# Kernel optimization log

Measured on AMD Instinct MI355X. Metric: run time of the kernel, lower is better.

## Reference

```python
import jax, jax.numpy as jnp
import numpy as np

K = 5  # kernel_size
B, N, H, Wd = 2, 8, 512, 512

def setup_inputs() -> dict:
    key = jax.random.key(0)
    k1, k2, k3 = jax.random.split(key, 3)
    frames = jax.random.normal(k1, (B, N, H, Wd), dtype=jnp.float32)
    core = jax.random.normal(k2, (B, N * K * K, H, Wd), dtype=jnp.float32)
    W = jax.random.uniform(k3, (B, N, H, Wd), dtype=jnp.float32)
    return {"frames": frames, "core": core, "W": W}

def reference(frames, core, W):
    b, n, h, w = frames.shape
    p = K // 2
    # pad spatial dims
    fp = jnp.pad(frames, ((0, 0), (0, 0), (p, p), (p, p)))
    # K^2 shifted views -> [B, N, K^2, H, W] (mirrors torch stack order i-major)
    patches = jnp.stack([fp[..., i:i + h, j:j + w] for i in range(K) for j in range(K)], axis=2)
    # split+stack of core along channels == reshape to [B, N, K^2, H, W]
    c = core.reshape(b, n, K * K, h, w)
    pred = jnp.sum(c * patches, axis=2)  # per-pixel dynamic conv
    return W * pred
```

## Files before the change

kernel.cpp:

```cpp
#include <hip/hip_runtime.h>


#define KK   5
#define PADR 2
#define BB   2
#define NN   8
#define HH   512
#define WW   512

constexpr int SROW    = WW + 2 * PADR;
constexpr int SSTRIDE = SROW + 4;

__global__ __launch_bounds__(128) void kpn_kernel(
    const float* __restrict__ frames,
    const float* __restrict__ core,
    const float* __restrict__ Wt,
    float* __restrict__ out)
{
    __shared__ float smem[KK * SSTRIDE];

    const int tid = threadIdx.x;
    const int h   = blockIdx.x % HH;
    const int bn  = blockIdx.x / HH;

    const float* fbase = frames + (size_t)bn * HH * WW;
    #pragma unroll
    for (int i = 0; i < KK; ++i) {
        const int  row = h - PADR + i;
        const bool rok = (row >= 0) && (row < HH);
        const float* frow = fbase + (size_t)row * WW;
        for (int idx = tid; idx < SROW; idx += 128) {
            const int x = idx - PADR;
            float v = 0.0f;
            if (rok && x >= 0 && x < WW) v = frow[x];
            smem[i * SSTRIDE + idx] = v;
        }
    }
    __syncthreads();

    const int w0 = tid * 4;

    float fr[KK][8];
    #pragma unroll
    for (int i = 0; i < KK; ++i) {
        #pragma unroll
        for (int t = 0; t < 8; ++t)
            fr[i][t] = smem[i * SSTRIDE + w0 + t];
    }

    float acc0 = 0.f, acc1 = 0.f, acc2 = 0.f, acc3 = 0.f;

    const float* cbase = core + ((size_t)bn * (KK * KK) * HH + h) * WW + w0;
    #pragma unroll
    for (int i = 0; i < KK; ++i) {
        #pragma unroll
        for (int j = 0; j < KK; ++j) {
            const int c = i * KK + j;
            const float4 cv = *(const float4*)(cbase + (size_t)c * HH * WW);
            acc0 += cv.x * fr[i][j + 0];
            acc1 += cv.y * fr[i][j + 1];
            acc2 += cv.z * fr[i][j + 2];
            acc3 += cv.w * fr[i][j + 3];
        }
    }

    const size_t o  = ((size_t)bn * HH + h) * WW + w0;
    const float4 wv = *(const float4*)(Wt + o);
    float4 ov;
    ov.x = wv.x * acc0;
    ov.y = wv.y * acc1;
    ov.z = wv.z * acc2;
    ov.w = wv.w * acc3;
    *(float4*)(out + o) = ov;
}

extern "C" void kernel_launch(void* const* d_in, const int* in_sizes, int n_in,
                              void* d_out, int out_size, void* d_ws, size_t ws_size,
                              hipStream_t stream)
{
    const float* frames = (const float*)d_in[0];
    const float* core   = (const float*)d_in[1];
    const float* Wt     = (const float*)d_in[2];
    float*       out    = (float*)d_out;

    const dim3 grid(BB * NN * HH);
    kpn_kernel<<<grid, 128, 0, stream>>>(frames, core, Wt, out);
}
```

Measured before the change: 569.2 us.

## Drop shared-memory staging; load frame halo directly with vector loads and nontemporal hints

Removes the shared-memory tile and barrier. Each thread now reads its own 8-wide halo per row straight from global memory using vector loads, so neighbouring threads' reads overlap and are served by cache. Streaming core and W reads and the output write use nontemporal loads and stores to reduce cache pollution. The grid becomes 2D, which removes the div/mod on the block index. The kernel is dominated by the core read bandwidth, so any gain is likely small. Redundant halo reads add some L1/L2 traffic.

```diff
diff --git a/kernel.cpp b/kernel.cpp
--- a/kernel.cpp
+++ b/kernel.cpp
@@ -2,14 +2,13 @@
 
 
 #define KK   5
-#define PADR 2
 #define BB   2
 #define NN   8
 #define HH   512
 #define WW   512
 
-constexpr int SROW    = WW + 2 * PADR;
-constexpr int SSTRIDE = SROW + 4;
+typedef float  v4f __attribute__((ext_vector_type(4)));
+typedef float  v2f __attribute__((ext_vector_type(2)));
 
 __global__ __launch_bounds__(128) void kpn_kernel(
     const float* __restrict__ frames,
@@ -17,61 +16,56 @@
     const float* __restrict__ Wt,
     float* __restrict__ out)
 {
-    __shared__ float smem[KK * SSTRIDE];
+    const int tid = threadIdx.x;
+    const int h   = blockIdx.x;
+    const int bn  = blockIdx.y;
+    const int w0  = tid * 4;
 
-    const int tid = threadIdx.x;
-    const int h   = blockIdx.x % HH;
-    const int bn  = blockIdx.x / HH;
+    const bool has_left  = (tid != 0);
+    const bool has_right = (tid != 127);
 
     const float* fbase = frames + (size_t)bn * HH * WW;
-    #pragma unroll
-    for (int i = 0; i < KK; ++i) {
-        const int  row = h - PADR + i;
-        const bool rok = (row >= 0) && (row < HH);
-        const float* frow = fbase + (size_t)row * WW;
-        for (int idx = tid; idx < SROW; idx += 128) {
-            const int x = idx - PADR;
-            float v = 0.0f;
-            if (rok && x >= 0 && x < WW) v = frow[x];
-            smem[i * SSTRIDE + idx] = v;
-        }
-    }
-    __syncthreads();
-
-    const int w0 = tid * 4;
-
-    float fr[KK][8];
-    #pragma unroll
-    for (int i = 0; i < KK; ++i) {
-        #pragma unroll
-        for (int t = 0; t < 8; ++t)
-            fr[i][t] = smem[i * SSTRIDE + w0 + t];
-    }
 
     float acc0 = 0.f, acc1 = 0.f, acc2 = 0.f, acc3 = 0.f;
 
     const float* cbase = core + ((size_t)bn * (KK * KK) * HH + h) * WW + w0;
+
     #pragma unroll
     for (int i = 0; i < KK; ++i) {
+        const int  r   = h - 2 + i;
+        const bool rok = (r >= 0) && (r < HH);
+        const float* rp = fbase + (size_t)r * WW + w0;
+
+        v2f a = {0.f, 0.f};
+        v4f b = {0.f, 0.f, 0.f, 0.f};
+        v2f c = {0.f, 0.f};
+        if (rok) {
+            b = *(const v4f*)(rp);
+            if (has_left)  a = *(const v2f*)(rp - 2);
+            if (has_right) c = *(const v2f*)(rp + 4);
+        }
+        const float frw[8] = {a.x, a.y, b.x, b.y, b.z, b.w, c.x, c.y};
+
         #pragma unroll
         for (int j = 0; j < KK; ++j) {
-            const int c = i * KK + j;
-            const float4 cv = *(const float4*)(cbase + (size_t)c * HH * WW);
-            acc0 += cv.x * fr[i][j + 0];
-            acc1 += cv.y * fr[i][j + 1];
-            acc2 += cv.z * fr[i][j + 2];
-            acc3 += cv.w * fr[i][j + 3];
+            const int ch = i * KK + j;
+            const v4f cv = __builtin_nontemporal_load(
+                (const v4f*)(cbase + (size_t)ch * HH * WW));
+            acc0 += cv.x * frw[j + 0];
+            acc1 += cv.y * frw[j + 1];
+            acc2 += cv.z * frw[j + 2];
+            acc3 += cv.w * frw[j + 3];
         }
     }
 
     const size_t o  = ((size_t)bn * HH + h) * WW + w0;
-    const float4 wv = *(const float4*)(Wt + o);
-    float4 ov;
+    const v4f wv = __builtin_nontemporal_load((const v4f*)(Wt + o));
+    v4f ov;
     ov.x = wv.x * acc0;
     ov.y = wv.y * acc1;
     ov.z = wv.z * acc2;
     ov.w = wv.w * acc3;
-    *(float4*)(out + o) = ov;
+    __builtin_nontemporal_store(ov, (v4f*)(out + o));
 }
 
 extern "C" void kernel_launch(void* const* d_in, const int* in_sizes, int n_in,
@@ -83,6 +77,6 @@
     const float* Wt     = (const float*)d_in[2];
     float*       out    = (float*)d_out;
 
-    const dim3 grid(BB * NN * HH);
+    dim3 grid(HH, BB * NN);
     kpn_kernel<<<grid, 128, 0, stream>>>(frames, core, Wt, out);
 }
```

Result: faster. 539.1 us (-5.3%).
